# Kernel tuning notes

Hardware: AMD Instinct MI355X
Metric: run time of the kernel (lower is better)

Reference implementation:

```python
import jax, jax.numpy as jnp
import numpy as np

_OFF = 8
_M = 512  # coordinate hash base (> max coord + 2*_OFF)

def _enc(c):
    c64 = c.astype(np.int64) + _OFF
    return (c64[:, 0] * _M + c64[:, 1]) * _M + c64[:, 2]

def _kmap(out_c, in_c, scale):
    """Per-offset neighbor map: maps[k, j] = index into in_c of voxel out_c[j] + scale*offset_k, or -1."""
    ik = _enc(in_c)
    order = np.argsort(ik)
    sk = ik[order]
    maps = np.full((27, len(out_c)), -1, np.int32)
    k = 0
    for dx in (-1, 0, 1):
        for dy in (-1, 0, 1):
            for dz in (-1, 0, 1):
                ck = _enc(out_c + np.array([dx, dy, dz]) * scale)
                pos = np.clip(np.searchsorted(sk, ck), 0, len(sk) - 1)
                hit = sk[pos] == ck
                maps[k] = np.where(hit, order[pos].astype(np.int32), -1)
                k += 1
    return maps


def setup_inputs() -> dict:
    rng = np.random.default_rng(0)
    c = rng.integers(0, 160, size=(300000, 3))
    c0 = np.unique(c, axis=0)[:200000]          # stride-1 voxels
    c2 = np.unique((c0 // 2) * 2, axis=0)       # stride-2 voxels
    c4 = np.unique((c2 // 4) * 4, axis=0)       # stride-4 voxels

    maps = {
        'map0':  jnp.asarray(_kmap(c0, c0, 1)),   # block0  (s=1)
        'map1':  jnp.asarray(_kmap(c2, c0, 1)),   # block1  (s=2 down)
        'map2':  jnp.asarray(_kmap(c4, c2, 2)),   # block2  (s=2 down)
        'map2t': jnp.asarray(_kmap(c2, c4, 2)),   # block2_tr (transposed)
        'map1t': jnp.asarray(_kmap(c0, c2, 1)),   # block1_tr (transposed)
        'map0t': jnp.asarray(_kmap(c0, c0, 1)),   # block0_tr (s=1)
    }

    key = jax.random.key(0)
    ks = jax.random.split(key, 8)

    def w(k, cin, cout):
        return jax.random.normal(k, (27, cin, cout), jnp.float32) / np.sqrt(27.0 * cin)

    nf, e = 16, 32
    inp = {'feats': jax.random.normal(ks[0], (c0.shape[0], nf), jnp.float32)}
    inp['W0'] = w(ks[1], nf, e);          inp['g0'] = jnp.ones((e,));        inp['b0'] = jnp.zeros((e,))
    inp['W1'] = w(ks[2], e, 2 * e);       inp['g1'] = jnp.ones((2 * e,));    inp['b1'] = jnp.zeros((2 * e,))
    inp['W2'] = w(ks[3], 2 * e, 4 * e);   inp['g2'] = jnp.ones((4 * e,));    inp['b2'] = jnp.zeros((4 * e,))
    inp['W2t'] = w(ks[4], 4 * e, 2 * e);  inp['g2t'] = jnp.ones((2 * e,));   inp['b2t'] = jnp.zeros((2 * e,))
    inp['W1t'] = w(ks[5], 4 * e, 2 * e);  inp['g1t'] = jnp.ones((2 * e,));   inp['b1t'] = jnp.zeros((2 * e,))
    inp['W0t'] = w(ks[6], 3 * e, 2)
    inp.update(maps)
    return inp


def _sconv(x, W, m):
    """Sparse 3D conv as gather-GEMM-scatter. x:[Nin,Cin], W:[27,Cin,Cout], m:[27,Nout]."""
    valid = m >= 0
    idx = jnp.maximum(m, 0)
    acc0 = jnp.zeros((m.shape[1], W.shape[2]), x.dtype)

    def body(acc, kw):
        mk, vk, Wk = kw
        g = jnp.where(vk[:, None], x[mk], 0.0)
        return acc + g @ Wk, None

    out, _ = jax.lax.scan(body, acc0, (idx, valid, W))
    return out


def _bn_relu(x, g, b, eps=1e-5):
    mu = x.mean(0)
    var = x.var(0)
    return jax.nn.relu((x - mu) * jax.lax.rsqrt(var + eps) * g + b)


def reference(feats, W0, g0, b0, W1, g1, b1, W2, g2, b2,
              W2t, g2t, b2t, W1t, g1t, b1t, W0t,
              map0, map1, map2, map2t, map1t, map0t):
    s1 = _bn_relu(_sconv(feats, W0, map0), g0, b0)   # [N0, 32]
    s2 = _bn_relu(_sconv(s1, W1, map1), g1, b1)      # [N1, 64]
    s4 = _bn_relu(_sconv(s2, W2, map2), g2, b2)      # [N2, 128]
    d2 = _bn_relu(_sconv(s4, W2t, map2t), g2t, b2t)  # [N1, 64]
    d2 = jnp.concatenate([d2, s2], axis=1)           # [N1, 128] skip cat
    d1 = _bn_relu(_sconv(d2, W1t, map1t), g1t, b1t)  # [N0, 64]
    d1 = jnp.concatenate([d1, s1], axis=1)           # [N0, 96] skip cat
    return _sconv(d1, W0t, map0t)                    # [N0, 2]
```

## Files before the change

kernel.cpp:

```cpp
#include <hip/hip_runtime.h>
#include <cstddef>
#include <cstdint>

#define BN_EPS 1e-5f

typedef float f2 __attribute__((ext_vector_type(2)));
typedef float f4 __attribute__((ext_vector_type(4)));
typedef float f32x4 __attribute__((ext_vector_type(4)));
typedef _Float16 h2 __attribute__((ext_vector_type(2)));
typedef _Float16 h8 __attribute__((ext_vector_type(8)));

__device__ __forceinline__ int xcd_swz(int bid, int nwg)
{
    const int q = nwg >> 3, r = nwg & 7;
    const int xcd = bid & 7, idx = bid >> 3;
    const int base = (xcd < r) ? xcd * (q + 1) : r * (q + 1) + (xcd - r) * q;
    return base + idx;
}

template<int CIN, int COUT>
__global__ __launch_bounds__(256)
void wtrans_mf(const float* __restrict__ W, _Float16* __restrict__ Wm)
{
    constexpr int NT = CIN / 32;
    constexpr int NC = COUT / 16;
    const int t = blockIdx.x * 256 + threadIdx.x;
    constexpr int TOTAL = 27 * NT * NC * 64;
    if (t >= TOTAL) return;
    const int lane = t & 63;
    int rest = t >> 6;
    const int ct = rest % NC; rest /= NC;
    const int tt = rest % NT;
    const int k  = rest / NT;
    const int cin0 = tt * 32 + (lane >> 4) * 8;
    const int co   = ct * 16 + (lane & 15);
    h8 v;
    #pragma unroll
    for (int u = 0; u < 8; ++u)
        v[u] = (_Float16)W[((size_t)k * CIN + cin0 + u) * COUT + co];
    *(h8*)(Wm + (size_t)t * 8) = v;
}

__global__ __launch_bounds__(256)
void wtrans_mf0(const float* __restrict__ W, _Float16* __restrict__ Wm0)
{
    const int t = blockIdx.x * 256 + threadIdx.x;
    constexpr int TOTAL = 27 * 2 * 32;
    if (t >= TOTAL) return;
    const int co = t % 32;
    const int s  = (t / 32) % 2;
    const int k  = t / 64;
    h8 v;
    #pragma unroll
    for (int u = 0; u < 8; ++u)
        v[u] = (_Float16)W[((size_t)k * 16 + s * 8 + u) * 32 + co];
    *(h8*)(Wm0 + (size_t)t * 8) = v;
}

__global__ __launch_bounds__(256)
void map_transpose_cls(const int* __restrict__ map, int Nout,
                       int* __restrict__ mapT, unsigned char* __restrict__ cls,
                       int* __restrict__ counts)
{
    __shared__ int s[256][28];
    __shared__ int hist[9];
    const int tid  = threadIdx.x;
    const int base = blockIdx.x * 256;
    const int j    = base + tid;
    if (tid < 9) hist[tid] = 0;
    for (int k = 0; k < 27; ++k)
        s[tid][k] = (j < Nout) ? map[(size_t)k * Nout + j] : -1;
    __syncthreads();
    for (int i = tid; i < 256 * 32; i += 256) {
        const int r = i >> 5, c = i & 31;
        if (base + r < Nout)
            mapT[(size_t)(base + r) * 32 + c] = (c < 27) ? s[r][c] : -1;
    }
    if (j < Nout) {
        int c9 = 8;
        #pragma unroll 1
        for (int k = 0; k < 27; ++k) {
            if (s[tid][k] >= 0) {
                const int dz = k % 3, dy = (k / 3) % 3, dx = k / 9;
                c9 = ((dx != 1) << 2) | ((dy != 1) << 1) | (int)(dz != 1);
                break;
            }
        }
        cls[j] = (unsigned char)c9;
        atomicAdd(&hist[c9], 1);
    }
    __syncthreads();
    if (tid < 9 && hist[tid] > 0)
        atomicAdd(&counts[tid], hist[tid]);
}

__global__ __launch_bounds__(256)
void scatter_compact(const unsigned char* __restrict__ cls, int Nout,
                     const int* __restrict__ counts, int* __restrict__ cursors,
                     int* __restrict__ order)
{
    __shared__ int hist[9], basec[9];
    const int tid = threadIdx.x;
    const int j   = blockIdx.x * 256 + tid;
    if (tid < 9) hist[tid] = 0;
    const int c9 = (j < Nout) ? (int)cls[j] : -1;
    __syncthreads();
    int lpos = 0;
    if (c9 >= 0) lpos = atomicAdd(&hist[c9], 1);
    __syncthreads();
    if (tid < 9 && hist[tid] > 0)
        basec[tid] = atomicAdd(&cursors[tid], hist[tid]);
    __syncthreads();
    if (c9 >= 0) {
        int offs = 0;
        #pragma unroll
        for (int c = 0; c < 9; ++c)
            if (c < c9) offs += counts[c];
        order[offs + basec[c9] + lpos] = j;
    }
}

__global__ __launch_bounds__(256)
void sconv_mf0(const float* __restrict__ x, const _Float16* __restrict__ Wm0,
               const int* __restrict__ map, int Nout,
               _Float16* __restrict__ out, const float* __restrict__ zrow)
{
    const int lane = threadIdx.x & 63;
    const int wave = threadIdx.x >> 6;
    const int row0 = (blockIdx.x * 4 + wave) * 16;

    __shared__ int smap[4][16][28];

    int mk[16];
    bool anyv = false;
    #pragma unroll
    for (int r = 0; r < 16; ++r) {
        const int j = row0 + r;
        mk[r] = (lane < 27 && j < Nout) ? map[(size_t)lane * Nout + j] : -1;
        anyv |= (mk[r] >= 0);
    }
    unsigned long long act = __ballot(anyv);

    if (lane < 27) {
        #pragma unroll
        for (int r = 0; r < 16; ++r)
            smap[wave][r][lane] = mk[r];
    }

    f32x4 accH[2], accL[2];
    #pragma unroll
    for (int c = 0; c < 2; ++c) {
        accH[c] = (f32x4){0.f, 0.f, 0.f, 0.f};
        accL[c] = (f32x4){0.f, 0.f, 0.f, 0.f};
    }

    const int rrow = lane & 15;
    const int kseg = lane >> 4;
    const int half = kseg & 1;
    const bool useK1 = (kseg < 2);

    while (act) {
        const int k1 = (int)__builtin_ctzll(act);
        act &= act - 1;
        int k2 = -1;
        if (act) {
            k2 = (int)__builtin_ctzll(act);
            act &= act - 1;
        }
        const int ks = useK1 ? k1 : k2;
        int m = -1;
        if (ks >= 0) m = smap[wave][rrow][ks];

        const float* px = (m >= 0) ? (x + (size_t)m * 16 + half * 8)
                                   : (zrow + half * 8);
        const f4 x0 = *(const f4*)px;
        const f4 x1 = *(const f4*)(px + 4);
        h8 aH, aL;
        #pragma unroll
        for (int u = 0; u < 4; ++u) {
            const float v0 = x0[u], v1 = x1[u];
            const _Float16 h0 = (_Float16)v0;
            const _Float16 h1 = (_Float16)v1;
            aH[u]     = h0;
            aH[u + 4] = h1;
            aL[u]     = (_Float16)((v0 - (float)h0) * 2048.f);
            aL[u + 4] = (_Float16)((v1 - (float)h1) * 2048.f);
        }

        const int ksafe = (ks >= 0) ? ks : 0;
        const _Float16* wb = Wm0 + ((size_t)(ksafe * 2 + half) * 32) * 8;
        #pragma unroll
        for (int c = 0; c < 2; ++c) {
            const h8 b = *(const h8*)(wb + (size_t)(c * 16 + rrow) * 8);
            accH[c] = __builtin_amdgcn_mfma_f32_16x16x32_f16(aH, b, accH[c], 0, 0, 0);
            accL[c] = __builtin_amdgcn_mfma_f32_16x16x32_f16(aL, b, accL[c], 0, 0, 0);
        }
    }

    #pragma unroll
    for (int c = 0; c < 2; ++c) {
        #pragma unroll
        for (int r = 0; r < 4; ++r) {
            const int j = row0 + kseg * 4 + r;
            if (j < Nout)
                out[(size_t)j * 32 + c * 16 + rrow] =
                    (_Float16)(accH[c][r] + accL[c][r] * (1.f / 2048.f));
        }
    }
}

template<int CIN, int CINA, int COUT, int NTILE>
__global__ __launch_bounds__(256)
void sconv_mf(const _Float16* __restrict__ xA, const _Float16* __restrict__ xB,
              const _Float16* __restrict__ Wm, const int* __restrict__ map,
              int Nout, _Float16* __restrict__ out,
              const _Float16* __restrict__ zrh)
{
    constexpr int CINB = CIN - CINA;
    constexpr int NT = CIN / 32;
    constexpr int NC = COUT / 16;
    constexpr int RPW = NTILE * 16;
    static_assert(CINA % 32 == 0, "CINA must be a multiple of 32");
    const int lane = threadIdx.x & 63;
    const int wave = threadIdx.x >> 6;
    const int row0 = (blockIdx.x * 4 + wave) * RPW;

    __shared__ int smap[4][RPW][28];

    int mv[RPW];
    #pragma unroll
    for (int r = 0; r < RPW; ++r) {
        const int j = row0 + r;
        mv[r] = (lane < 27 && j < Nout) ? map[(size_t)lane * Nout + j] : -1;
    }
    bool anyv = false;
    #pragma unroll
    for (int r = 0; r < RPW; ++r) {
        if (lane < 27) smap[wave][r][lane] = mv[r];
        anyv |= (mv[r] >= 0);
    }
    unsigned long long act = __ballot(anyv) & 0x7FFFFFFull;

    f32x4 acc[NTILE][NC];
    #pragma unroll
    for (int tt = 0; tt < NTILE; ++tt)
        #pragma unroll
        for (int c = 0; c < NC; ++c) acc[tt][c] = (f32x4){0.f, 0.f, 0.f, 0.f};

    const int rrow = lane & 15;
    const int kseg = lane >> 4;

    auto loada = [&](int k, h8 a[NTILE][NT]) {
        #pragma unroll
        for (int tt = 0; tt < NTILE; ++tt) {
            const int m = smap[wave][tt * 16 + rrow][k];
            #pragma unroll
            for (int t = 0; t < NT; ++t) {
                const int cin0 = t * 32 + kseg * 8;
                const _Float16* pa;
                if (m >= 0) {
                    if (CINB > 0 && t * 32 >= CINA)
                        pa = xB + (size_t)m * CINB + (cin0 - CINA);
                    else
                        pa = xA + (size_t)m * CINA + cin0;
                } else {
                    pa = zrh;
                }
                a[tt][t] = *(const h8*)pa;
            }
        }
    };
    auto compute = [&](int k, h8 a[NTILE][NT]) {
        const _Float16* Wk = Wm + ((size_t)k * NT * NC * 64 + lane) * 8;
        #pragma unroll
        for (int t = 0; t < NT; ++t) {
            #pragma unroll
            for (int c = 0; c < NC; ++c) {
                const h8 b = *(const h8*)(Wk + (size_t)(t * NC + c) * 64 * 8);
                #pragma unroll
                for (int tt = 0; tt < NTILE; ++tt)
                    acc[tt][c] = __builtin_amdgcn_mfma_f32_16x16x32_f16(a[tt][t], b, acc[tt][c], 0, 0, 0);
            }
        }
    };

    h8 aC[NTILE][NT], aN[NTILE][NT];
    int kC = -1;
    if (act) {
        kC = (int)__builtin_ctzll(act);
        act &= act - 1;
        loada(kC, aC);
    }
    while (kC >= 0) {
        int kN = -1;
        if (act) {
            kN = (int)__builtin_ctzll(act);
            act &= act - 1;
            loada(kN, aN);
        }
        compute(kC, aC);
        #pragma unroll
        for (int tt = 0; tt < NTILE; ++tt)
            #pragma unroll
            for (int t = 0; t < NT; ++t) aC[tt][t] = aN[tt][t];
        kC = kN;
    }

    #pragma unroll
    for (int tt = 0; tt < NTILE; ++tt) {
        #pragma unroll
        for (int c = 0; c < NC; ++c) {
            #pragma unroll
            for (int r = 0; r < 4; ++r) {
                const int j = row0 + tt * 16 + kseg * 4 + r;
                if (j < Nout)
                    out[(size_t)j * COUT + c * 16 + rrow] = (_Float16)acc[tt][c][r];
            }
        }
    }
}

template<int CIN, int CINA, int COUT>
__global__ __launch_bounds__(256)
void sconv_mf_g(const _Float16* __restrict__ xA, const _Float16* __restrict__ xB,
                const _Float16* __restrict__ Wm, const int* __restrict__ mapT,
                const int* __restrict__ order, int Nout,
                _Float16* __restrict__ out, const _Float16* __restrict__ zrh)
{
    constexpr int CINB = CIN - CINA;
    constexpr int NT = CIN / 32;
    constexpr int NC = COUT / 16;
    static_assert(CINA % 32 == 0, "CINA must be a multiple of 32");
    const int lane = threadIdx.x & 63;
    const int wave = threadIdx.x >> 6;
    const int wrow0 = (blockIdx.x * 4 + wave) * 32;

    __shared__ int sjr[4][32];
    __shared__ int smap[4][32][28];

    int jreg = -1;
    if (lane < 32) {
        const int idx = wrow0 + lane;
        if (idx < Nout) jreg = order[idx];
    }
    if (!__ballot(jreg >= 0)) return;
    if (lane < 32) sjr[wave][lane] = jreg;

    int mv[32];
    #pragma unroll
    for (int r = 0; r < 32; ++r) {
        const int jr = __shfl(jreg, r);
        mv[r] = (jr >= 0 && lane < 27) ? mapT[(size_t)jr * 32 + lane] : -1;
    }
    bool anyv = false;
    #pragma unroll
    for (int r = 0; r < 32; ++r) {
        if (lane < 27) smap[wave][r][lane] = mv[r];
        anyv |= (mv[r] >= 0);
    }
    unsigned long long act = __ballot(anyv) & 0x7FFFFFFull;

    f32x4 acc[2][NC];
    #pragma unroll
    for (int tt = 0; tt < 2; ++tt)
        #pragma unroll
        for (int c = 0; c < NC; ++c) acc[tt][c] = (f32x4){0.f, 0.f, 0.f, 0.f};

    const int rrow = lane & 15;
    const int kseg = lane >> 4;

    auto loada = [&](int k, h8 a[2][NT]) {
        #pragma unroll
        for (int tt = 0; tt < 2; ++tt) {
            const int m = smap[wave][tt * 16 + rrow][k];
            #pragma unroll
            for (int t = 0; t < NT; ++t) {
                const int cin0 = t * 32 + kseg * 8;
                const _Float16* pa;
                if (m >= 0) {
                    if (CINB > 0 && t * 32 >= CINA)
                        pa = xB + (size_t)m * CINB + (cin0 - CINA);
                    else
                        pa = xA + (size_t)m * CINA + cin0;
                } else {
                    pa = zrh;
                }
                a[tt][t] = *(const h8*)pa;
            }
        }
    };
    auto compute = [&](int k, h8 a[2][NT]) {
        const _Float16* Wk = Wm + ((size_t)k * NT * NC * 64 + lane) * 8;
        #pragma unroll
        for (int t = 0; t < NT; ++t) {
            #pragma unroll
            for (int c = 0; c < NC; ++c) {
                const h8 b = *(const h8*)(Wk + (size_t)(t * NC + c) * 64 * 8);
                acc[0][c] = __builtin_amdgcn_mfma_f32_16x16x32_f16(a[0][t], b, acc[0][c], 0, 0, 0);
                acc[1][c] = __builtin_amdgcn_mfma_f32_16x16x32_f16(a[1][t], b, acc[1][c], 0, 0, 0);
            }
        }
    };

    h8 aC[2][NT], aN[2][NT];
    int kC = -1;
    if (act) {
        kC = (int)__builtin_ctzll(act);
        act &= act - 1;
        loada(kC, aC);
    }
    while (kC >= 0) {
        int kN = -1;
        if (act) {
            kN = (int)__builtin_ctzll(act);
            act &= act - 1;
            loada(kN, aN);
        }
        compute(kC, aC);
        #pragma unroll
        for (int tt = 0; tt < 2; ++tt)
            #pragma unroll
            for (int t = 0; t < NT; ++t) aC[tt][t] = aN[tt][t];
        kC = kN;
    }

    #pragma unroll
    for (int tt = 0; tt < 2; ++tt) {
        #pragma unroll
        for (int c = 0; c < NC; ++c) {
            #pragma unroll
            for (int r = 0; r < 4; ++r) {
                const int j = sjr[wave][tt * 16 + kseg * 4 + r];
                if (j >= 0)
                    out[(size_t)j * COUT + c * 16 + rrow] = (_Float16)acc[tt][c][r];
            }
        }
    }
}

__global__ __launch_bounds__(256)
void sconv0t(const _Float16* __restrict__ d1, const _Float16* __restrict__ s1,
             const float* __restrict__ W ,
             const int* __restrict__ map, int N, float* __restrict__ out,
             const _Float16* __restrict__ zrh)
{
    const int tid  = threadIdx.x;
    const int lane = tid & 63;
    const int l32  = tid & 31;
    const int bid  = xcd_swz(blockIdx.x, gridDim.x);
    const int j    = bid * 8 + (tid >> 5);

    int mk = (l32 < 27 && j < N) ? map[(size_t)l32 * N + j] : -1;
    const unsigned long long bal = __ballot(mk >= 0);
    unsigned int act = (unsigned int)((bal | (bal >> 32)) & 0x7FFFFFFu);

    float a0 = 0.f, a1 = 0.f;
    while (act) {
        const int k1 = (int)__builtin_ctz(act);
        act &= act - 1;
        int k2 = -1;
        if (act) { k2 = (int)__builtin_ctz(act); act &= act - 1; }
        const int k2s = (k2 >= 0) ? k2 : k1;

        const int m1 = __shfl(mk, (lane & 32) + k1);
        int m2 = __shfl(mk, (lane & 32) + k2s);
        if (k2 < 0) m2 = -1;

        const _Float16* p1a = (m1 >= 0) ? (d1 + (size_t)m1 * 64) : zrh;
        const _Float16* p1b = (m1 >= 0) ? (s1 + (size_t)m1 * 32) : zrh;
        const _Float16* p2a = (m2 >= 0) ? (d1 + (size_t)m2 * 64) : zrh;
        const _Float16* p2b = (m2 >= 0) ? (s1 + (size_t)m2 * 32) : zrh;
        const h2 xa1 = *(const h2*)(p1a + 2 * l32);
        const float xs1 = (float)p1b[l32];
        const h2 xa2 = *(const h2*)(p2a + 2 * l32);
        const float xs2 = (float)p2b[l32];

        const f4 wa1 = *(const f4*)(W + (size_t)k1 * 192 + 4 * l32);
        const f2 ws1 = *(const f2*)(W + (size_t)k1 * 192 + 128 + 2 * l32);
        const f4 wa2 = *(const f4*)(W + (size_t)k2s * 192 + 4 * l32);
        const f2 ws2 = *(const f2*)(W + (size_t)k2s * 192 + 128 + 2 * l32);

        a0 = fmaf((float)xa1[0], wa1[0], a0);
        a1 = fmaf((float)xa1[0], wa1[1], a1);
        a0 = fmaf((float)xa1[1], wa1[2], a0);
        a1 = fmaf((float)xa1[1], wa1[3], a1);
        a0 = fmaf(xs1, ws1[0], a0);
        a1 = fmaf(xs1, ws1[1], a1);

        a0 = fmaf((float)xa2[0], wa2[0], a0);
        a1 = fmaf((float)xa2[0], wa2[1], a1);
        a0 = fmaf((float)xa2[1], wa2[2], a0);
        a1 = fmaf((float)xa2[1], wa2[3], a1);
        a0 = fmaf(xs2, ws2[0], a0);
        a1 = fmaf(xs2, ws2[1], a1);
    }
    #pragma unroll
    for (int off = 1; off < 32; off <<= 1) {
        a0 += __shfl_xor(a0, off, 32);
        a1 += __shfl_xor(a1, off, 32);
    }
    if (l32 == 0 && j < N) {
        out[(size_t)j * 2 + 0] = a0;
        out[(size_t)j * 2 + 1] = a1;
    }
}

template<int C>
__global__ __launch_bounds__(256)
void bn_reduce_v(const _Float16* __restrict__ x, int N,
                 float* __restrict__ sums)
{
    constexpr int CV = C / 8;
    const int tid  = threadIdx.x;
    const int lane = tid & 63;
    const int wave = tid >> 6;
    const size_t total  = (size_t)N * CV;
    const size_t stride = (size_t)gridDim.x * 256;
    const size_t gid    = (size_t)blockIdx.x * 256 + tid;

    float s[8], s2[8];
    #pragma unroll
    for (int u = 0; u < 8; ++u) { s[u] = 0.f; s2[u] = 0.f; }

    for (size_t v = gid; v < total; v += stride) {
        const h8 hv = *(const h8*)(x + v * 8);
        #pragma unroll
        for (int u = 0; u < 8; ++u) {
            const float f = (float)hv[u];
            s[u] += f;
            s2[u] += f * f;
        }
    }

    #pragma unroll
    for (int off = CV; off < 64; off <<= 1) {
        #pragma unroll
        for (int u = 0; u < 8; ++u) {
            s[u]  += __shfl_xor(s[u], off);
            s2[u] += __shfl_xor(s2[u], off);
        }
    }

    __shared__ float shs[4][16][8];
    __shared__ float shq[4][16][8];
    if (lane < CV) {
        #pragma unroll
        for (int u = 0; u < 8; ++u) {
            shs[wave][lane][u] = s[u];
            shq[wave][lane][u] = s2[u];
        }
    }
    __syncthreads();
    if (tid < C) {
        const int ph = tid >> 3, u = tid & 7;
        float ts = 0.f, tq = 0.f;
        #pragma unroll
        for (int w = 0; w < 4; ++w) {
            ts += shs[w][ph][u];
            tq += shq[w][ph][u];
        }
        atomicAdd(&sums[tid], ts);
        atomicAdd(&sums[C + tid], tq);
    }
}

template<int C>
__global__ __launch_bounds__(256)
void bn_apply_v(_Float16* __restrict__ x, int N,
                const float* __restrict__ sums,
                const float* __restrict__ g, const float* __restrict__ b)
{
    constexpr int CV = C / 8;
    const size_t total  = (size_t)N * CV;
    const size_t stride = (size_t)gridDim.x * 256;
    const size_t gid    = (size_t)blockIdx.x * 256 + threadIdx.x;
    const int phase = (int)(gid % CV);

    const float invN = 1.0f / (float)N;
    float sc[8], sh[8];
    #pragma unroll
    for (int u = 0; u < 8; ++u) {
        const int c = phase * 8 + u;
        const float mean = sums[c] * invN;
        float var = sums[C + c] * invN - mean * mean;
        var = fmaxf(var, 0.f);
        sc[u] = g[c] * rsqrtf(var + BN_EPS);
        sh[u] = b[c] - mean * sc[u];
    }

    for (size_t v = gid; v < total; v += stride) {
        h8 hv = *(h8*)(x + v * 8);
        #pragma unroll
        for (int u = 0; u < 8; ++u) {
            const float f = fmaf((float)hv[u], sc[u], sh[u]);
            hv[u] = (_Float16)(f > 0.f ? f : 0.f);
        }
        *(h8*)(x + v * 8) = hv;
    }
}

extern "C" void kernel_launch(void* const* d_in, const int* in_sizes, int n_in,
                              void* d_out, int out_size, void* d_ws, size_t ws_size,
                              hipStream_t stream)
{
    const float* feats = (const float*)d_in[0];
    const float* W0  = (const float*)d_in[1];
    const float* g0  = (const float*)d_in[2];
    const float* b0  = (const float*)d_in[3];
    const float* W1  = (const float*)d_in[4];
    const float* g1  = (const float*)d_in[5];
    const float* b1  = (const float*)d_in[6];
    const float* W2  = (const float*)d_in[7];
    const float* g2  = (const float*)d_in[8];
    const float* b2  = (const float*)d_in[9];
    const float* W2t = (const float*)d_in[10];
    const float* g2t = (const float*)d_in[11];
    const float* b2t = (const float*)d_in[12];
    const float* W1t = (const float*)d_in[13];
    const float* g1t = (const float*)d_in[14];
    const float* b1t = (const float*)d_in[15];
    const float* W0t = (const float*)d_in[16];
    const int* map0  = (const int*)d_in[17];
    const int* map1  = (const int*)d_in[18];
    const int* map2  = (const int*)d_in[19];
    const int* map2t = (const int*)d_in[20];
    const int* map1t = (const int*)d_in[21];
    const int* map0t = (const int*)d_in[22];

    const int N0 = in_sizes[0] / 16;
    const int N1 = in_sizes[18] / 27;
    const int N2 = in_sizes[19] / 27;

    float* ws = (float*)d_ws;
    float* sums  = ws;
    float* sums0 = sums;
    float* sums1 = sums + 64;
    float* sums2 = sums + 192;
    float* sums3 = sums + 448;
    float* sums4 = sums + 576;
    float* zrow  = sums + 704;
    int*   gcnt  = (int*)(zrow + 128);
    _Float16* Wm0h = (_Float16*)(gcnt + 64);
    _Float16* Wh1  = Wm0h + 27 * 2 * 32 * 8;
    _Float16* Wh2  = Wh1 + 27 * 32 * 64;
    _Float16* Wh2t = Wh2 + 27 * 64 * 128;
    _Float16* Wh1t = Wh2t + 27 * 128 * 64;
    _Float16* y0 = Wh1t + 27 * 128 * 64;
    _Float16* y1 = y0 + (size_t)N0 * 32;
    _Float16* y2 = y1 + (size_t)N1 * 64;
    _Float16* y3 = y2 + (size_t)N2 * 128;
    _Float16* y4 = y3 + (size_t)N1 * 64;
    int* mapT = (int*)(y4 + (size_t)N0 * 64);
    int* orderA = mapT + (size_t)N0 * 32;
    int* orderB = orderA + N1;
    unsigned char* clsb = (unsigned char*)(orderB + N0);
    const _Float16* zrh = (const _Float16*)zrow;

    (void)hipMemsetAsync(sums, 0, (704 + 128 + 64) * sizeof(float), stream);

    wtrans_mf0<<<(27 * 2 * 32 + 255) / 256, 256, 0, stream>>>(W0, Wm0h);
    wtrans_mf<32, 64><<<(27 * 1 * 4 * 64 + 255) / 256, 256, 0, stream>>>(W1, Wh1);
    wtrans_mf<64, 128><<<(27 * 2 * 8 * 64 + 255) / 256, 256, 0, stream>>>(W2, Wh2);
    wtrans_mf<128, 64><<<(27 * 4 * 4 * 64 + 255) / 256, 256, 0, stream>>>(W2t, Wh2t);
    wtrans_mf<128, 64><<<(27 * 4 * 4 * 64 + 255) / 256, 256, 0, stream>>>(W1t, Wh1t);

    sconv_mf0<<<(N0 + 63) / 64, 256, 0, stream>>>(
        feats, Wm0h, map0, N0, y0, zrow);
    bn_reduce_v<32><<<512, 256, 0, stream>>>(y0, N0, sums0);
    bn_apply_v<32><<<1024, 256, 0, stream>>>(y0, N0, sums0, g0, b0);

    sconv_mf<32, 32, 64, 2><<<(N1 + 127) / 128, 256, 0, stream>>>(
        y0, nullptr, Wh1, map1, N1, y1, zrh);
    bn_reduce_v<64><<<512, 256, 0, stream>>>(y1, N1, sums1);
    bn_apply_v<64><<<1024, 256, 0, stream>>>(y1, N1, sums1, g1, b1);

    sconv_mf<64, 64, 128, 1><<<(N2 + 63) / 64, 256, 0, stream>>>(
        y1, nullptr, Wh2, map2, N2, y2, zrh);
    bn_reduce_v<128><<<512, 256, 0, stream>>>(y2, N2, sums2);
    bn_apply_v<128><<<1024, 256, 0, stream>>>(y2, N2, sums2, g2, b2);

    map_transpose_cls<<<(N1 + 255) / 256, 256, 0, stream>>>(
        map2t, N1, mapT, clsb, gcnt);
    scatter_compact<<<(N1 + 255) / 256, 256, 0, stream>>>(
        clsb, N1, gcnt, gcnt + 16, orderA);
    sconv_mf_g<128, 128, 64><<<(N1 + 127) / 128, 256, 0, stream>>>(
        y2, nullptr, Wh2t, mapT, orderA, N1, y3, zrh);
    bn_reduce_v<64><<<512, 256, 0, stream>>>(y3, N1, sums3);
    bn_apply_v<64><<<1024, 256, 0, stream>>>(y3, N1, sums3, g2t, b2t);

    map_transpose_cls<<<(N0 + 255) / 256, 256, 0, stream>>>(
        map1t, N0, mapT, clsb, gcnt + 32);
    scatter_compact<<<(N0 + 255) / 256, 256, 0, stream>>>(
        clsb, N0, gcnt + 32, gcnt + 48, orderB);
    sconv_mf_g<128, 64, 64><<<(N0 + 127) / 128, 256, 0, stream>>>(
        y3, y1, Wh1t, mapT, orderB, N0, y4, zrh);
    bn_reduce_v<64><<<512, 256, 0, stream>>>(y4, N0, sums4);
    bn_apply_v<64><<<1024, 256, 0, stream>>>(y4, N0, sums4, g1t, b1t);

    sconv0t<<<(N0 + 7) / 8, 256, 0, stream>>>(y4, y0, W0t, map0t, N0,
                                              (float*)d_out, zrh);
}
```

Before: 629.7 us.

## Fuse batch-norm statistic reduction into sparse conv epilogues

Each sparse-convolution kernel now accumulates per-channel sum and sum-of-squares of its fp16 outputs in the epilogue. It reduces them across lanes with shuffles, then through shared-memory atomics, and adds them to the global sums with atomics. The five separate bn_reduce_v launches, which re-read each activation tensor, are removed. The early-return in the gather kernel is dropped so that every thread reaches the barriers, at the cost of extra epilogue work and global atomics per block.

Measured after the change: 659.4 us. 4.7% more time.

```diff
diff --git a/kernel.cpp b/kernel.cpp
--- a/kernel.cpp
+++ b/kernel.cpp
@@ -123,13 +123,18 @@
 __global__ __launch_bounds__(256)
 void sconv_mf0(const float* __restrict__ x, const _Float16* __restrict__ Wm0,
                const int* __restrict__ map, int Nout,
-               _Float16* __restrict__ out, const float* __restrict__ zrow)
-{
-    const int lane = threadIdx.x & 63;
-    const int wave = threadIdx.x >> 6;
+               _Float16* __restrict__ out, const float* __restrict__ zrow,
+               float* __restrict__ sums)
+{
+    const int tid  = threadIdx.x;
+    const int lane = tid & 63;
+    const int wave = tid >> 6;
     const int row0 = (blockIdx.x * 4 + wave) * 16;
 
     __shared__ int smap[4][16][28];
+    __shared__ float bsum[2][32];
+
+    if (tid < 32) { bsum[0][tid] = 0.f; bsum[1][tid] = 0.f; }
 
     int mk[16];
     bool anyv = false;
@@ -197,15 +202,44 @@
         }
     }
 
+    float ps[2], pq[2];
+    #pragma unroll
+    for (int c = 0; c < 2; ++c) { ps[c] = 0.f; pq[c] = 0.f; }
+
     #pragma unroll
     for (int c = 0; c < 2; ++c) {
         #pragma unroll
         for (int r = 0; r < 4; ++r) {
             const int j = row0 + kseg * 4 + r;
+            const _Float16 hv =
+                (_Float16)(accH[c][r] + accL[c][r] * (1.f / 2048.f));
             if (j < Nout)
-                out[(size_t)j * 32 + c * 16 + rrow] =
-                    (_Float16)(accH[c][r] + accL[c][r] * (1.f / 2048.f));
-        }
+                out[(size_t)j * 32 + c * 16 + rrow] = hv;
+            const float v = (float)hv;
+            ps[c] += v;
+            pq[c] += v * v;
+        }
+    }
+    #pragma unroll
+    for (int off = 16; off < 64; off <<= 1) {
+        #pragma unroll
+        for (int c = 0; c < 2; ++c) {
+            ps[c] += __shfl_xor(ps[c], off);
+            pq[c] += __shfl_xor(pq[c], off);
+        }
+    }
+    __syncthreads();
+    if (lane < 16) {
+        #pragma unroll
+        for (int c = 0; c < 2; ++c) {
+            atomicAdd(&bsum[0][c * 16 + rrow], ps[c]);
+            atomicAdd(&bsum[1][c * 16 + rrow], pq[c]);
+        }
+    }
+    __syncthreads();
+    if (tid < 32) {
+        atomicAdd(&sums[tid], bsum[0][tid]);
+        atomicAdd(&sums[32 + tid], bsum[1][tid]);
     }
 }
 
@@ -214,18 +248,22 @@
 void sconv_mf(const _Float16* __restrict__ xA, const _Float16* __restrict__ xB,
               const _Float16* __restrict__ Wm, const int* __restrict__ map,
               int Nout, _Float16* __restrict__ out,
-              const _Float16* __restrict__ zrh)
+              const _Float16* __restrict__ zrh, float* __restrict__ sums)
 {
     constexpr int CINB = CIN - CINA;
     constexpr int NT = CIN / 32;
     constexpr int NC = COUT / 16;
     constexpr int RPW = NTILE * 16;
     static_assert(CINA % 32 == 0, "CINA must be a multiple of 32");
-    const int lane = threadIdx.x & 63;
-    const int wave = threadIdx.x >> 6;
+    const int tid  = threadIdx.x;
+    const int lane = tid & 63;
+    const int wave = tid >> 6;
     const int row0 = (blockIdx.x * 4 + wave) * RPW;
 
     __shared__ int smap[4][RPW][28];
+    __shared__ float bsum[2][COUT];
+
+    if (tid < COUT) { bsum[0][tid] = 0.f; bsum[1][tid] = 0.f; }
 
     int mv[RPW];
     #pragma unroll
@@ -306,6 +344,10 @@
         kC = kN;
     }
 
+    float ps[NC], pq[NC];
+    #pragma unroll
+    for (int c = 0; c < NC; ++c) { ps[c] = 0.f; pq[c] = 0.f; }
+
     #pragma unroll
     for (int tt = 0; tt < NTILE; ++tt) {
         #pragma unroll
@@ -313,10 +355,35 @@
             #pragma unroll
             for (int r = 0; r < 4; ++r) {
                 const int j = row0 + tt * 16 + kseg * 4 + r;
+                const _Float16 hv = (_Float16)acc[tt][c][r];
                 if (j < Nout)
-                    out[(size_t)j * COUT + c * 16 + rrow] = (_Float16)acc[tt][c][r];
+                    out[(size_t)j * COUT + c * 16 + rrow] = hv;
+                const float v = (float)hv;
+                ps[c] += v;
+                pq[c] += v * v;
             }
         }
+    }
+    #pragma unroll
+    for (int off = 16; off < 64; off <<= 1) {
+        #pragma unroll
+        for (int c = 0; c < NC; ++c) {
+            ps[c] += __shfl_xor(ps[c], off);
+            pq[c] += __shfl_xor(pq[c], off);
+        }
+    }
+    __syncthreads();
+    if (lane < 16) {
+        #pragma unroll
+        for (int c = 0; c < NC; ++c) {
+            atomicAdd(&bsum[0][c * 16 + rrow], ps[c]);
+            atomicAdd(&bsum[1][c * 16 + rrow], pq[c]);
+        }
+    }
+    __syncthreads();
+    if (tid < COUT) {
+        atomicAdd(&sums[tid], bsum[0][tid]);
+        atomicAdd(&sums[COUT + tid], bsum[1][tid]);
     }
 }
 
@@ -325,25 +392,29 @@
 void sconv_mf_g(const _Float16* __restrict__ xA, const _Float16* __restrict__ xB,
                 const _Float16* __restrict__ Wm, const int* __restrict__ mapT,
                 const int* __restrict__ order, int Nout,
-                _Float16* __restrict__ out, const _Float16* __restrict__ zrh)
+                _Float16* __restrict__ out, const _Float16* __restrict__ zrh,
+                float* __restrict__ sums)
 {
     constexpr int CINB = CIN - CINA;
     constexpr int NT = CIN / 32;
     constexpr int NC = COUT / 16;
     static_assert(CINA % 32 == 0, "CINA must be a multiple of 32");
-    const int lane = threadIdx.x & 63;
-    const int wave = threadIdx.x >> 6;
+    const int tid  = threadIdx.x;
+    const int lane = tid & 63;
+    const int wave = tid >> 6;
     const int wrow0 = (blockIdx.x * 4 + wave) * 32;
 
     __shared__ int sjr[4][32];
     __shared__ int smap[4][32][28];
+    __shared__ float bsum[2][COUT];
+
+    if (tid < COUT) { bsum[0][tid] = 0.f; bsum[1][tid] = 0.f; }
 
     int jreg = -1;
     if (lane < 32) {
         const int idx = wrow0 + lane;
         if (idx < Nout) jreg = order[idx];
     }
-    if (!__ballot(jreg >= 0)) return;
     if (lane < 32) sjr[wave][lane] = jreg;
 
     int mv[32];
@@ -424,6 +495,10 @@
         kC = kN;
     }
 
+    float ps[NC], pq[NC];
+    #pragma unroll
+    for (int c = 0; c < NC; ++c) { ps[c] = 0.f; pq[c] = 0.f; }
+
     #pragma unroll
     for (int tt = 0; tt < 2; ++tt) {
         #pragma unroll
@@ -431,10 +506,35 @@
             #pragma unroll
             for (int r = 0; r < 4; ++r) {
                 const int j = sjr[wave][tt * 16 + kseg * 4 + r];
+                const _Float16 hv = (_Float16)acc[tt][c][r];
                 if (j >= 0)
-                    out[(size_t)j * COUT + c * 16 + rrow] = (_Float16)acc[tt][c][r];
+                    out[(size_t)j * COUT + c * 16 + rrow] = hv;
+                const float v = (float)hv;
+                ps[c] += v;
+                pq[c] += v * v;
             }
         }
+    }
+    #pragma unroll
+    for (int off = 16; off < 64; off <<= 1) {
+        #pragma unroll
+        for (int c = 0; c < NC; ++c) {
+            ps[c] += __shfl_xor(ps[c], off);
+            pq[c] += __shfl_xor(pq[c], off);
+        }
+    }
+    __syncthreads();
+    if (lane < 16) {
+        #pragma unroll
+        for (int c = 0; c < NC; ++c) {
+            atomicAdd(&bsum[0][c * 16 + rrow], ps[c]);
+            atomicAdd(&bsum[1][c * 16 + rrow], pq[c]);
+        }
+    }
+    __syncthreads();
+    if (tid < COUT) {
+        atomicAdd(&sums[tid], bsum[0][tid]);
+        atomicAdd(&sums[COUT + tid], bsum[1][tid]);
     }
 }
 
@@ -502,65 +602,6 @@
     if (l32 == 0 && j < N) {
         out[(size_t)j * 2 + 0] = a0;
         out[(size_t)j * 2 + 1] = a1;
-    }
-}
-
-template<int C>
-__global__ __launch_bounds__(256)
-void bn_reduce_v(const _Float16* __restrict__ x, int N,
-                 float* __restrict__ sums)
-{
-    constexpr int CV = C / 8;
-    const int tid  = threadIdx.x;
-    const int lane = tid & 63;
-    const int wave = tid >> 6;
-    const size_t total  = (size_t)N * CV;
-    const size_t stride = (size_t)gridDim.x * 256;
-    const size_t gid    = (size_t)blockIdx.x * 256 + tid;
-
-    float s[8], s2[8];
-    #pragma unroll
-    for (int u = 0; u < 8; ++u) { s[u] = 0.f; s2[u] = 0.f; }
-
-    for (size_t v = gid; v < total; v += stride) {
-        const h8 hv = *(const h8*)(x + v * 8);
-        #pragma unroll
-        for (int u = 0; u < 8; ++u) {
-            const float f = (float)hv[u];
-            s[u] += f;
-            s2[u] += f * f;
-        }
-    }
-
-    #pragma unroll
-    for (int off = CV; off < 64; off <<= 1) {
-        #pragma unroll
-        for (int u = 0; u < 8; ++u) {
-            s[u]  += __shfl_xor(s[u], off);
-            s2[u] += __shfl_xor(s2[u], off);
-        }
-    }
-
-    __shared__ float shs[4][16][8];
-    __shared__ float shq[4][16][8];
-    if (lane < CV) {
-        #pragma unroll
-        for (int u = 0; u < 8; ++u) {
-            shs[wave][lane][u] = s[u];
-            shq[wave][lane][u] = s2[u];
-        }
-    }
-    __syncthreads();
-    if (tid < C) {
-        const int ph = tid >> 3, u = tid & 7;
-        float ts = 0.f, tq = 0.f;
-        #pragma unroll
-        for (int w = 0; w < 4; ++w) {
-            ts += shs[w][ph][u];
-            tq += shq[w][ph][u];
-        }
-        atomicAdd(&sums[tid], ts);
-        atomicAdd(&sums[C + tid], tq);
     }
 }
 
@@ -665,18 +706,15 @@
     wtrans_mf<128, 64><<<(27 * 4 * 4 * 64 + 255) / 256, 256, 0, stream>>>(W1t, Wh1t);
 
     sconv_mf0<<<(N0 + 63) / 64, 256, 0, stream>>>(
-        feats, Wm0h, map0, N0, y0, zrow);
-    bn_reduce_v<32><<<512, 256, 0, stream>>>(y0, N0, sums0);
+        feats, Wm0h, map0, N0, y0, zrow, sums0);
     bn_apply_v<32><<<1024, 256, 0, stream>>>(y0, N0, sums0, g0, b0);
 
     sconv_mf<32, 32, 64, 2><<<(N1 + 127) / 128, 256, 0, stream>>>(
-        y0, nullptr, Wh1, map1, N1, y1, zrh);
-    bn_reduce_v<64><<<512, 256, 0, stream>>>(y1, N1, sums1);
+        y0, nullptr, Wh1, map1, N1, y1, zrh, sums1);
     bn_apply_v<64><<<1024, 256, 0, stream>>>(y1, N1, sums1, g1, b1);
 
     sconv_mf<64, 64, 128, 1><<<(N2 + 63) / 64, 256, 0, stream>>>(
-        y1, nullptr, Wh2, map2, N2, y2, zrh);
-    bn_reduce_v<128><<<512, 256, 0, stream>>>(y2, N2, sums2);
+        y1, nullptr, Wh2, map2, N2, y2, zrh, sums2);
     bn_apply_v<128><<<1024, 256, 0, stream>>>(y2, N2, sums2, g2, b2);
 
     map_transpose_cls<<<(N1 + 255) / 256, 256, 0, stream>>>(
@@ -684,8 +722,7 @@
     scatter_compact<<<(N1 + 255) / 256, 256, 0, stream>>>(
         clsb, N1, gcnt, gcnt + 16, orderA);
     sconv_mf_g<128, 128, 64><<<(N1 + 127) / 128, 256, 0, stream>>>(
-        y2, nullptr, Wh2t, mapT, orderA, N1, y3, zrh);
-    bn_reduce_v<64><<<512, 256, 0, stream>>>(y3, N1, sums3);
+        y2, nullptr, Wh2t, mapT, orderA, N1, y3, zrh, sums3);
     bn_apply_v<64><<<1024, 256, 0, stream>>>(y3, N1, sums3, g2t, b2t);
 
     map_transpose_cls<<<(N0 + 255) / 256, 256, 0, stream>>>(
@@ -693,8 +730,7 @@
     scatter_compact<<<(N0 + 255) / 256, 256, 0, stream>>>(
         clsb, N0, gcnt + 32, gcnt + 48, orderB);
     sconv_mf_g<128, 64, 64><<<(N0 + 127) / 128, 256, 0, stream>>>(
-        y3, y1, Wh1t, mapT, orderB, N0, y4, zrh);
-    bn_reduce_v<64><<<512, 256, 0, stream>>>(y4, N0, sums4);
+        y3, y1, Wh1t, mapT, orderB, N0, y4, zrh, sums4);
     bn_apply_v<64><<<1024, 256, 0, stream>>>(y4, N0, sums4, g1t, b1t);
 
     sconv0t<<<(N0 + 7) / 8, 256, 0, stream>>>(y4, y0, W0t, map0t, N0,
```
